# Kernel tuning notes

Hardware: AMD Instinct MI355X
Metric: run time of the kernel (lower is better)

The kernel has to match this reference:

```python
import jax, jax.numpy as jnp
import numpy as np

B, S, N, C, D = 1, 6, 10000, 128, 4
HEADS, PTS = 4, 8
HF, WF = 28, 50
M = HF * WF


def setup_inputs() -> dict:
    key0 = jax.random.key(0)
    ks = jax.random.split(key0, 14)
    sc = C ** -0.5
    d = {}
    d["query"] = jax.random.normal(ks[0], (B, N, C), jnp.float32)
    d["key"] = jax.random.normal(ks[1], (S, M, B, C), jnp.float32)
    d["value"] = jax.random.normal(ks[2], (S, M, B, C), jnp.float32)
    d["query_pos"] = jax.random.normal(ks[3], (B, N, C), jnp.float32) * 0.1
    d["reference_points_cam"] = jax.random.uniform(ks[4], (S, B, N, D, 2), jnp.float32, -0.2, 1.2)
    d["bev_mask"] = jax.random.randint(ks[5], (S, B, N, D), 0, 2).astype(bool)
    d["w_off"] = jax.random.normal(ks[6], (C, HEADS * PTS * 2), jnp.float32) * sc
    d["b_off"] = jax.random.normal(ks[7], (HEADS * PTS * 2,), jnp.float32) * 0.01
    d["w_attn"] = jax.random.normal(ks[8], (C, HEADS * PTS), jnp.float32) * sc
    d["b_attn"] = jax.random.normal(ks[9], (HEADS * PTS,), jnp.float32) * 0.01
    d["w_val"] = jax.random.normal(ks[10], (C, C), jnp.float32) * sc
    d["b_val"] = jax.random.normal(ks[11], (C,), jnp.float32) * 0.01
    d["w_out"] = jax.random.normal(ks[12], (C, C), jnp.float32) * sc
    d["b_out"] = jax.random.normal(ks[13], (C,), jnp.float32) * 0.01
    d["Hf"] = HF
    d["Wf"] = WF
    return d


def reference(query, key, value, query_pos, reference_points_cam, bev_mask,
              w_off, b_off, w_attn, b_attn, w_val, b_val, w_out, b_out, Hf, Wf):
    # SpatialCrossAttention with MSDeformAttn3D (BEVFormer semantics, eval mode: dropout=identity).
    # The torch data-dependent gather/rebatch/scatter is replaced by mathematically equivalent
    # masked computation: deformable attention is per-query independent, so running it for all
    # BEV queries per camera and mask-accumulating yields identical slots.
    B_, N_, C_ = query.shape
    S_ = key.shape[0]
    D_ = reference_points_cam.shape[3]
    H, P = HEADS, PTS
    dh = C_ // H
    Pd = P // D_
    q = query + query_pos  # (B,N,C)
    off = (q @ w_off + b_off).reshape(B_, N_, H, Pd, D_, 2)
    aw = jax.nn.softmax((q @ w_attn + b_attn).reshape(B_, N_, H, P), axis=-1)  # over levels*points (L=1)
    # value projection; per-camera feature maps laid out as (B,S,H,Hf*Wf,dh)
    v = jnp.transpose(value, (2, 0, 1, 3))  # (B,S,M,C)
    v = v @ w_val + b_val
    v = v.reshape(B_, S_, Hf * Wf, H, dh).transpose(0, 1, 3, 2, 4)  # (B,S,H,M,dh)
    ref = jnp.transpose(reference_points_cam, (1, 0, 2, 3, 4))  # (B,S,N,D,2)
    norm = jnp.array([Wf, Hf], jnp.float32)  # offset_normalizer = (W, H)
    loc = ref[:, :, :, None, None, :, :] + off[:, None] / norm  # (B,S,N,H,Pd,D,2)
    loc = loc.reshape(B_, S_, N_, H, P, 2)
    # bilinear sampling, zero padding, align_corners=False
    ix = loc[..., 0] * Wf - 0.5
    iy = loc[..., 1] * Hf - 0.5
    x0 = jnp.floor(ix)
    y0 = jnp.floor(iy)

    def flat(a):  # (B,S,N,H,P) -> (B,S,H,N*P)
        return a.transpose(0, 1, 3, 2, 4).reshape(B_, S_, H, N_ * P)

    def gather(xi, yi):
        ok = (xi >= 0) & (xi < Wf) & (yi >= 0) & (yi < Hf)
        xi_c = jnp.clip(xi, 0, Wf - 1).astype(jnp.int32)
        yi_c = jnp.clip(yi, 0, Hf - 1).astype(jnp.int32)
        idx = flat(yi_c * Wf + xi_c)
        g = jnp.take_along_axis(v, idx[..., None], axis=3)  # (B,S,H,N*P,dh)
        return g * flat(ok.astype(v.dtype))[..., None]

    wx1 = ix - x0
    wy1 = iy - y0
    wx0 = 1.0 - wx1
    wy0 = 1.0 - wy1
    samp = (gather(x0, y0) * flat(wx0 * wy0)[..., None]
            + gather(x0 + 1, y0) * flat(wx1 * wy0)[..., None]
            + gather(x0, y0 + 1) * flat(wx0 * wy1)[..., None]
            + gather(x0 + 1, y0 + 1) * flat(wx1 * wy1)[..., None])  # (B,S,H,N*P,dh)
    samp = samp.reshape(B_, S_, H, N_, P, dh)
    out = jnp.einsum('bshnpd,bnhp->bsnhd', samp, aw).reshape(B_, S_, N_, C_)
    # masked scatter-accumulate back to BEV slots
    mask = jnp.transpose(jnp.any(bev_mask, axis=-1), (1, 0, 2))  # (B,S,N)
    slots = jnp.sum(out * mask[..., None].astype(out.dtype), axis=1)  # (B,N,C)
    count = jnp.maximum(mask.astype(out.dtype).sum(axis=1), 1.0)
    slots = slots / count[..., None]
    return slots @ w_out + b_out + query  # dropout is identity in eval
```

## Files before the change

### kernel.cpp

```cpp
#include <hip/hip_runtime.h>
#include <math.h>

#define S_ 6
#define N_ 10000
#define C_ 128
#define D_ 4
#define H_ 4
#define P_ 8
#define HF_ 28
#define WF_ 50
#define M_ (HF_ * WF_)
#define DH_ 32
#define SM_ (S_ * M_)
#define ABYTES (S_ * H_ * M_ * 32)
#define VB_SH (M_ * 32)
#define CQ 64
#define NCH ((N_ + CQ - 1) / CQ)

#define NB_V ((SM_ + 31) / 32)
#define NB_O ((N_ + 31) / 32)

typedef float floatx2 __attribute__((ext_vector_type(2)));

template <int NC, int MT, int MR, int MODE>
__device__ __forceinline__ void gemm_body(
    const float* __restrict__ A, const float* __restrict__ A2,
    const float* __restrict__ B0, const float* __restrict__ B1,
    const float* __restrict__ bias0, const float* __restrict__ bias1,
    float* __restrict__ outf, char* __restrict__ out8,
    int Mrows, int m0, int tid, int nthreads, float (*Alds)[132]) {
  constexpr int NTHR = (NC / 4) * (MT / MR);

  for (int i = tid; i < MT * 32; i += nthreads) {
    int r = i >> 5, k = (i & 31) * 4;
    int row = m0 + r;
    float4 v = make_float4(0.f, 0.f, 0.f, 0.f);
    if (row < Mrows) {
      v = *(const float4*)(A + (size_t)row * C_ + k);
      if (MODE == 1) {
        float4 v2 = *(const float4*)(A2 + (size_t)row * C_ + k);
        v.x += v2.x; v.y += v2.y; v.z += v2.z; v.w += v2.w;
      }
    }
    *(float4*)(&Alds[r][k]) = v;
  }
  __syncthreads();
  if (tid >= NTHR) return;

  int ci = tid % (NC / 4);
  int mi = tid / (NC / 4);
  int c0 = ci * 4, r0 = mi * MR;

  const float* bs;
  if (MODE == 1) bs = (c0 < 64) ? bias0 + c0 : bias1 + (c0 - 64);
  else bs = bias0 + c0;

  float acc[MR][4];
#pragma unroll
  for (int j = 0; j < MR; ++j)
#pragma unroll
    for (int cc = 0; cc < 4; ++cc) acc[j][cc] = bs[cc];

#pragma unroll 2
  for (int k4 = 0; k4 < C_; k4 += 4) {
    float bf[16];
#pragma unroll
    for (int kk = 0; kk < 4; ++kk) {
      int k = k4 + kk;
      float4 b4;
      if (MODE == 1)
        b4 = (c0 < 64) ? *(const float4*)(B0 + (size_t)k * 64 + c0)
                       : *(const float4*)(B1 + (size_t)k * 32 + (c0 - 64));
      else
        b4 = *(const float4*)(B0 + (size_t)k * NC + c0);
      bf[kk * 4 + 0] = b4.x; bf[kk * 4 + 1] = b4.y;
      bf[kk * 4 + 2] = b4.z; bf[kk * 4 + 3] = b4.w;
    }
    float af[MR * 4];
#pragma unroll
    for (int j = 0; j < MR; ++j) {
      float4 a4 = *(const float4*)(&Alds[r0 + j][k4]);
      af[j * 4 + 0] = a4.x; af[j * 4 + 1] = a4.y;
      af[j * 4 + 2] = a4.z; af[j * 4 + 3] = a4.w;
    }
#pragma unroll
    for (int j = 0; j < MR; ++j)
#pragma unroll
      for (int kk = 0; kk < 4; ++kk)
#pragma unroll
        for (int cc = 0; cc < 4; ++cc)
          acc[j][cc] = fmaf(af[j * 4 + kk], bf[kk * 4 + cc], acc[j][cc]);
  }

#pragma unroll
  for (int j = 0; j < MR; ++j) {
    int row = m0 + r0 + j;
    if (row >= Mrows) continue;
    if (MODE == 0) {
      int mm = row % M_;
      int h = c0 >> 5, d0 = c0 & 31;
      int s = row / M_;
      int w = __builtin_amdgcn_cvt_pk_fp8_f32(acc[j][0], acc[j][1], 0, false);
      w = __builtin_amdgcn_cvt_pk_fp8_f32(acc[j][2], acc[j][3], w, true);
      size_t hm = (size_t)s * H_ + h;
      *(int*)(out8 + (hm * M_ + mm) * 32 + d0) = w;
    } else if (MODE == 1) {
      *(float4*)(outf + (size_t)row * 96 + c0) =
          make_float4(acc[j][0], acc[j][1], acc[j][2], acc[j][3]);
    }
  }
}

__global__ __launch_bounds__(256) void prep_kernel(
    const float* __restrict__ value, const float* __restrict__ w_val,
    const float* __restrict__ b_val, char* __restrict__ vh8,
    const float* __restrict__ query, const float* __restrict__ query_pos,
    const float* __restrict__ w_off, const float* __restrict__ b_off,
    const float* __restrict__ w_attn, const float* __restrict__ b_attn,
    float* __restrict__ OFFL) {
  __shared__ float Alds[32][132];
  int bid = blockIdx.x;
  if (bid < NB_V) {
    gemm_body<128, 32, 4, 0>(value, nullptr, w_val, nullptr, b_val, nullptr,
                             nullptr, vh8, SM_, bid * 32, threadIdx.x, 256,
                             Alds);
  } else {
    gemm_body<96, 32, 4, 1>(query, query_pos, w_off, w_attn, b_off, b_attn,
                            OFFL, nullptr, N_, (bid - NB_V) * 32, threadIdx.x,
                            256, Alds);
  }
}

__global__ __launch_bounds__(512, 4) void attn5_kernel(
    const float* __restrict__ OFFL,
    const float* __restrict__ refpts,
    const int*   __restrict__ bev_mask,
    const char*  __restrict__ wsbase,
    float* __restrict__ slot) {
  __shared__ int4 Vl4[M_ * 2];
  __shared__ int4 Pp[CQ * 9];

  int bid = blockIdx.x;
  int h = bid & 3;
  int q0 = (bid >> 2) * CQ;
  int tid = threadIdx.x;

  int tp = tid & 7, tq = tid >> 3;
  int qP = q0 + tq;
  int qPc = (qP < N_) ? qP : (N_ - 1);

  int w = tid >> 6, lane = tid & 63;
  int qg = lane >> 3, c8 = lane & 7;
  int rowsel = (c8 >> 2) & 1, xsel = (c8 >> 1) & 1, chalf = c8 & 1;
  int xsh = xsel << 4;
  int ql = w * 8 + qg;
  int qG = q0 + ql;
  int qGvalid = (qG < N_);

  float aw_p, offx, offy;
  {
    const float* lg = OFFL + (size_t)qPc * 96 + 64 + h * 8;
    float4 l0 = *(const float4*)(lg + 0);
    float4 l1 = *(const float4*)(lg + 4);
    float e[8] = {l0.x, l0.y, l0.z, l0.w, l1.x, l1.y, l1.z, l1.w};
    float mx = -1e30f;
#pragma unroll
    for (int p = 0; p < 8; ++p) mx = fmaxf(mx, e[p]);
    float sum = 0.f;
#pragma unroll
    for (int p = 0; p < 8; ++p) { e[p] = expf(e[p] - mx); sum += e[p]; }
    aw_p = e[tp] / sum;
    int pd = tp >> 2, dd = tp & 3;
    const float* ob = OFFL + (size_t)qPc * 96 + h * 16 + pd * 8 + dd * 2;
    offx = ob[0]; offy = ob[1];
  }

  floatx2 acc[8] = {{0.f, 0.f}, {0.f, 0.f}, {0.f, 0.f}, {0.f, 0.f},
                    {0.f, 0.f}, {0.f, 0.f}, {0.f, 0.f}, {0.f, 0.f}};

  for (int s = 0; s < S_; ++s) {
    __syncthreads();

    {
      const char* gsrc = wsbase + 64 + (size_t)(s * H_ + h) * VB_SH;
#pragma unroll
      for (int r = 0; r < 6; ++r) {
        int i = r * 512 + tid;
        if (i < M_ * 2) {
          __builtin_amdgcn_global_load_lds(
              (const __attribute__((address_space(1))) unsigned int*)(gsrc +
                                                                      i * 16),
              (__attribute__((address_space(3))) unsigned int*)&Vl4[i], 16, 0,
              0);
        }
      }
    }

    {
      int dd = tp & 3;
      const float* rf = refpts + ((size_t)s * N_ + qPc) * 8 + dd * 2;
      float rx = rf[0], ry = rf[1];
      const int* bm = bev_mask + ((size_t)s * N_ + qPc) * D_;
      int4 bmv = *(const int4*)bm;
      float A = ((bmv.x | bmv.y | bmv.z | bmv.w) ? 1.f : 0.f) * aw_p;
      float ix = rx * (float)WF_ + offx - 0.5f;
      float iy = ry * (float)HF_ + offy - 0.5f;
      float xf = floorf(ix), yf = floorf(iy);
      int x0 = (int)xf, y0 = (int)yf;
      float fx = ix - xf, fy = iy - yf;
      float gx = 1.f - fx, gy = 1.f - fy;
      bool vx0 = (x0 >= 0) && (x0 < WF_);
      bool vx1 = (x0 >= -1) && (x0 < WF_ - 1);
      bool vy0 = (y0 >= 0) && (y0 < HF_);
      bool vy1 = (y0 >= -1) && (y0 < HF_ - 1);
      float w00 = (vx0 && vy0) ? gx * gy * A : 0.f;
      float w10 = (vx1 && vy0) ? fx * gy * A : 0.f;
      float w01 = (vx0 && vy1) ? gx * fy * A : 0.f;
      float w11 = (vx1 && vy1) ? fx * fy * A : 0.f;
      int yt = min(max(y0, 0), HF_ - 1) * WF_;
      int yb = min(max(y0 + 1, 0), HF_ - 1) * WF_;
      int xc0 = min(max(x0, 0), WF_ - 1);
      int xc1 = min(max(x0 + 1, 0), WF_ - 1);
      int4 pk;
      pk.x = ((yt + xc0) * 2) | (((yt + xc1) * 2) << 16);
      pk.y = ((yb + xc0) * 2) | (((yb + xc1) * 2) << 16);
      union { _Float16 hf[2]; int iv; } u01, u23;
      u01.hf[0] = (_Float16)w00; u01.hf[1] = (_Float16)w10;
      u23.hf[0] = (_Float16)w01; u23.hf[1] = (_Float16)w11;
      pk.z = u01.iv;
      pk.w = u23.iv;
      Pp[tq * 9 + tp] = pk;
    }
    __syncthreads();

#pragma unroll
    for (int p = 0; p < 8; ++p) {
      int4 prm = Pp[ql * 9 + p];
      int vword = rowsel ? prm.y : prm.x;
      int vidx = (int)(((unsigned)vword >> xsh) & 0xffffu);
      int wword = rowsel ? prm.w : prm.z;
      union { unsigned short u; _Float16 hf; } cu;
      cu.u = (unsigned short)((unsigned)wword >> xsh);
      float wgt = (float)cu.hf;
      int4 tv = Vl4[vidx + chalf];
      floatx2 wv = {wgt, wgt};
      acc[0] += __builtin_amdgcn_cvt_pk_f32_fp8(tv.x, false) * wv;
      acc[1] += __builtin_amdgcn_cvt_pk_f32_fp8(tv.x, true)  * wv;
      acc[2] += __builtin_amdgcn_cvt_pk_f32_fp8(tv.y, false) * wv;
      acc[3] += __builtin_amdgcn_cvt_pk_f32_fp8(tv.y, true)  * wv;
      acc[4] += __builtin_amdgcn_cvt_pk_f32_fp8(tv.z, false) * wv;
      acc[5] += __builtin_amdgcn_cvt_pk_f32_fp8(tv.z, true)  * wv;
      acc[6] += __builtin_amdgcn_cvt_pk_f32_fp8(tv.w, false) * wv;
      acc[7] += __builtin_amdgcn_cvt_pk_f32_fp8(tv.w, true)  * wv;
    }
  }

  float av[16];
#pragma unroll
  for (int k = 0; k < 8; ++k) { av[2 * k] = acc[k][0]; av[2 * k + 1] = acc[k][1]; }
#pragma unroll
  for (int k = 0; k < 16; ++k) av[k] += __shfl_xor(av[k], 2);
#pragma unroll
  for (int k = 0; k < 16; ++k) av[k] += __shfl_xor(av[k], 4);

  if (c8 < 2 && qGvalid) {
    int cnt = 0;
#pragma unroll
    for (int s = 0; s < S_; ++s) {
      const int* bm = bev_mask + ((size_t)s * N_ + qG) * D_;
      int4 bmv = *(const int4*)bm;
      cnt += (bmv.x | bmv.y | bmv.z | bmv.w) ? 1 : 0;
    }
    float inv = 1.f / (float)(cnt > 0 ? cnt : 1);
    float* dst = slot + (size_t)qG * C_ + h * DH_ + chalf * 16;
    *(float4*)(dst + 0)  = make_float4(av[0] * inv, av[1] * inv, av[2] * inv, av[3] * inv);
    *(float4*)(dst + 4)  = make_float4(av[4] * inv, av[5] * inv, av[6] * inv, av[7] * inv);
    *(float4*)(dst + 8)  = make_float4(av[8] * inv, av[9] * inv, av[10] * inv, av[11] * inv);
    *(float4*)(dst + 12) = make_float4(av[12] * inv, av[13] * inv, av[14] * inv, av[15] * inv);
  }
}

__global__ __launch_bounds__(256) void outproj_kernel(
    const float* __restrict__ slot, const float* __restrict__ query,
    const float* __restrict__ w_out, const float* __restrict__ b_out,
    float* __restrict__ out) {
  __shared__ float slds[32][132];
  int q0 = blockIdx.x * 32, tid = threadIdx.x;

  for (int i = tid; i < 32 * 32; i += 256) {
    int r = i >> 5, k = (i & 31) * 4;
    int qc = min(q0 + r, N_ - 1);
    *(float4*)(&slds[r][k]) = *(const float4*)(slot + (size_t)qc * C_ + k);
  }
  __syncthreads();

  {
    int ci = tid & 31, mi = tid >> 5;
    int c0 = ci * 4, r0 = mi * 4;
    float acc[4][4];
#pragma unroll
    for (int j = 0; j < 4; ++j) {
      int qq = min(q0 + r0 + j, N_ - 1);
      float4 qv = *(const float4*)(query + (size_t)qq * C_ + c0);
      float4 bv = *(const float4*)(b_out + c0);
      acc[j][0] = bv.x + qv.x; acc[j][1] = bv.y + qv.y;
      acc[j][2] = bv.z + qv.z; acc[j][3] = bv.w + qv.w;
    }
#pragma unroll 2
    for (int k4 = 0; k4 < C_; k4 += 4) {
      float bf[16];
#pragma unroll
      for (int kk = 0; kk < 4; ++kk) {
        float4 b4 = *(const float4*)(w_out + (size_t)(k4 + kk) * C_ + c0);
        bf[kk * 4 + 0] = b4.x; bf[kk * 4 + 1] = b4.y;
        bf[kk * 4 + 2] = b4.z; bf[kk * 4 + 3] = b4.w;
      }
      float af[16];
#pragma unroll
      for (int j = 0; j < 4; ++j) {
        float4 a4 = *(const float4*)(&slds[r0 + j][k4]);
        af[j * 4 + 0] = a4.x; af[j * 4 + 1] = a4.y;
        af[j * 4 + 2] = a4.z; af[j * 4 + 3] = a4.w;
      }
#pragma unroll
      for (int j = 0; j < 4; ++j)
#pragma unroll
        for (int kk = 0; kk < 4; ++kk)
#pragma unroll
          for (int cc = 0; cc < 4; ++cc)
            acc[j][cc] = fmaf(af[j * 4 + kk], bf[kk * 4 + cc], acc[j][cc]);
    }
#pragma unroll
    for (int j = 0; j < 4; ++j) {
      int qq = q0 + r0 + j;
      if (qq < N_)
        *(float4*)(out + (size_t)qq * C_ + c0) =
            make_float4(acc[j][0], acc[j][1], acc[j][2], acc[j][3]);
    }
  }
}

extern "C" void kernel_launch(void* const* d_in, const int* in_sizes, int n_in,
                              void* d_out, int out_size, void* d_ws, size_t ws_size,
                              hipStream_t stream) {
  const float* query     = (const float*)d_in[0];
  const float* value     = (const float*)d_in[2];
  const float* query_pos = (const float*)d_in[3];
  const float* refpts    = (const float*)d_in[4];
  const int*   bev_mask  = (const int*)d_in[5];
  const float* w_off     = (const float*)d_in[6];
  const float* b_off     = (const float*)d_in[7];
  const float* w_attn    = (const float*)d_in[8];
  const float* b_attn    = (const float*)d_in[9];
  const float* w_val     = (const float*)d_in[10];
  const float* b_val     = (const float*)d_in[11];
  const float* w_out     = (const float*)d_in[12];
  const float* b_out     = (const float*)d_in[13];

  char* ws = (char*)d_ws;
  char* vh8   = ws + 64;
  float* OFFL = (float*)(ws + 64 + 2 * (size_t)ABYTES + 64);
  float* SLOT = (float*)(ws + 64 + 2 * (size_t)ABYTES + 64 +
                         (size_t)N_ * 96 * 4);

  prep_kernel<<<NB_V + NB_O, 256, 0, stream>>>(
      value, w_val, b_val, vh8, query, query_pos, w_off, b_off, w_attn, b_attn,
      OFFL);
  attn5_kernel<<<NCH * H_, 512, 0, stream>>>(OFFL, refpts, bev_mask, ws, SLOT);
  outproj_kernel<<<(N_ + 31) / 32, 256, 0, stream>>>(SLOT, query, w_out, b_out,
                                                     (float*)d_out);
}
```

Before: 158.3 us.

## Double-buffer per-camera value staging and split channel halves across blocks

Restructures the attention kernel so each block handles one channel half of one head, with 256 threads instead of 512. Camera feature maps and packed sample parameters are double-buffered in LDS, so the next camera's global-to-LDS load and parameter computation overlap with the current camera's accumulation, removing one barrier per iteration. The cost is twice as many blocks, each recomputing the softmax and offsets for its queries, along with strided 16-byte loads and a different shuffle reduction. The smaller per-block LDS staging may also change occupancy.

```diff
diff --git a/kernel.cpp b/kernel.cpp
--- a/kernel.cpp
+++ b/kernel.cpp
@@ -131,143 +131,173 @@
   }
 }
 
-__global__ __launch_bounds__(512, 4) void attn5_kernel(
+__global__ __launch_bounds__(256, 2) void attn6_kernel(
     const float* __restrict__ OFFL,
     const float* __restrict__ refpts,
     const int*   __restrict__ bev_mask,
     const char*  __restrict__ wsbase,
     float* __restrict__ slot) {
-  __shared__ int4 Vl4[M_ * 2];
-  __shared__ int4 Pp[CQ * 9];
+  __shared__ int4 Vbuf[2][M_];
+  __shared__ int4 Pp[2][CQ * 9];
 
   int bid = blockIdx.x;
-  int h = bid & 3;
-  int q0 = (bid >> 2) * CQ;
+  int chalf = bid & 1;
+  int h = (bid >> 1) & 3;
+  int q0 = (bid >> 3) * CQ;
   int tid = threadIdx.x;
 
-  int tp = tid & 7, tq = tid >> 3;
-  int qP = q0 + tq;
-  int qPc = (qP < N_) ? qP : (N_ - 1);
-
   int w = tid >> 6, lane = tid & 63;
-  int qg = lane >> 3, c8 = lane & 7;
-  int rowsel = (c8 >> 2) & 1, xsel = (c8 >> 1) & 1, chalf = c8 & 1;
+  int role = lane & 3, ql16 = lane >> 2;
+  int rowsel = role >> 1, xsel = role & 1;
   int xsh = xsel << 4;
-  int ql = w * 8 + qg;
-  int qG = q0 + ql;
-  int qGvalid = (qG < N_);
-
-  float aw_p, offx, offy;
+  int qlG = w * 16 + ql16;
+  int qG = q0 + qlG;
+  bool qGv = (qG < N_);
+  int qGc = qGv ? qG : (N_ - 1);
+
+  int pA = tid & 7, qA = tid >> 3;
+  int gqA = min(q0 + qA, N_ - 1);
+  int gqB = min(q0 + qA + 32, N_ - 1);
+
+  float awA, oxA, oyA, awB, oxB, oyB;
   {
-    const float* lg = OFFL + (size_t)qPc * 96 + 64 + h * 8;
-    float4 l0 = *(const float4*)(lg + 0);
-    float4 l1 = *(const float4*)(lg + 4);
-    float e[8] = {l0.x, l0.y, l0.z, l0.w, l1.x, l1.y, l1.z, l1.w};
+    const float* lg = OFFL + (size_t)gqA * 96 + 64 + h * 8;
+    float e[8];
     float mx = -1e30f;
 #pragma unroll
-    for (int p = 0; p < 8; ++p) mx = fmaxf(mx, e[p]);
+    for (int p = 0; p < 8; ++p) { e[p] = lg[p]; mx = fmaxf(mx, e[p]); }
     float sum = 0.f;
 #pragma unroll
     for (int p = 0; p < 8; ++p) { e[p] = expf(e[p] - mx); sum += e[p]; }
-    aw_p = e[tp] / sum;
-    int pd = tp >> 2, dd = tp & 3;
-    const float* ob = OFFL + (size_t)qPc * 96 + h * 16 + pd * 8 + dd * 2;
-    offx = ob[0]; offy = ob[1];
-  }
+    awA = e[pA] / sum;
+    int pd = pA >> 2, dd = pA & 3;
+    const float* ob = OFFL + (size_t)gqA * 96 + h * 16 + pd * 8 + dd * 2;
+    oxA = ob[0]; oyA = ob[1];
+  }
+  {
+    const float* lg = OFFL + (size_t)gqB * 96 + 64 + h * 8;
+    float e[8];
+    float mx = -1e30f;
+#pragma unroll
+    for (int p = 0; p < 8; ++p) { e[p] = lg[p]; mx = fmaxf(mx, e[p]); }
+    float sum = 0.f;
+#pragma unroll
+    for (int p = 0; p < 8; ++p) { e[p] = expf(e[p] - mx); sum += e[p]; }
+    awB = e[pA] / sum;
+    int pd = pA >> 2, dd = pA & 3;
+    const float* ob = OFFL + (size_t)gqB * 96 + h * 16 + pd * 8 + dd * 2;
+    oxB = ob[0]; oyB = ob[1];
+  }
+
+  auto stage = [&](int s) {
+    int b = s & 1;
+    const char* gsrc = wsbase + 64 + (size_t)(s * H_ + h) * VB_SH + chalf * 16;
+#pragma unroll
+    for (int r = 0; r < 6; ++r) {
+      int i = r * 256 + tid;
+      if (i < M_) {
+        __builtin_amdgcn_global_load_lds(
+            (const __attribute__((address_space(1))) unsigned int*)(gsrc +
+                                                                    (size_t)i *
+                                                                        32),
+            (__attribute__((address_space(3))) unsigned int*)&Vbuf[b][i], 16,
+            0, 0);
+      }
+    }
+  };
+
+  auto psample = [&](int s, int b, int gq, int qloc, int p, float aw, float ox,
+                     float oy) {
+    int dd = p & 3;
+    const float* rf = refpts + ((size_t)s * N_ + gq) * 8 + dd * 2;
+    float rx = rf[0], ry = rf[1];
+    const int* bm = bev_mask + ((size_t)s * N_ + gq) * D_;
+    int4 bmv = *(const int4*)bm;
+    float A = ((bmv.x | bmv.y | bmv.z | bmv.w) ? 1.f : 0.f) * aw;
+    float ix = rx * (float)WF_ + ox - 0.5f;
+    float iy = ry * (float)HF_ + oy - 0.5f;
+    float xf = floorf(ix), yf = floorf(iy);
+    int x0 = (int)xf, y0 = (int)yf;
+    float fx = ix - xf, fy = iy - yf;
+    float gx = 1.f - fx, gy = 1.f - fy;
+    bool vx0 = (x0 >= 0) && (x0 < WF_);
+    bool vx1 = (x0 >= -1) && (x0 < WF_ - 1);
+    bool vy0 = (y0 >= 0) && (y0 < HF_);
+    bool vy1 = (y0 >= -1) && (y0 < HF_ - 1);
+    float w00 = (vx0 && vy0) ? gx * gy * A : 0.f;
+    float w10 = (vx1 && vy0) ? fx * gy * A : 0.f;
+    float w01 = (vx0 && vy1) ? gx * fy * A : 0.f;
+    float w11 = (vx1 && vy1) ? fx * fy * A : 0.f;
+    int yt = min(max(y0, 0), HF_ - 1) * WF_;
+    int yb = min(max(y0 + 1, 0), HF_ - 1) * WF_;
+    int xc0 = min(max(x0, 0), WF_ - 1);
+    int xc1 = min(max(x0 + 1, 0), WF_ - 1);
+    int4 pk;
+    pk.x = (yt + xc0) | ((yt + xc1) << 16);
+    pk.y = (yb + xc0) | ((yb + xc1) << 16);
+    union { _Float16 hf[2]; int iv; } u01, u23;
+    u01.hf[0] = (_Float16)w00; u01.hf[1] = (_Float16)w10;
+    u23.hf[0] = (_Float16)w01; u23.hf[1] = (_Float16)w11;
+    pk.z = u01.iv;
+    pk.w = u23.iv;
+    Pp[b][qloc * 9 + p] = pk;
+  };
 
   floatx2 acc[8] = {{0.f, 0.f}, {0.f, 0.f}, {0.f, 0.f}, {0.f, 0.f},
                     {0.f, 0.f}, {0.f, 0.f}, {0.f, 0.f}, {0.f, 0.f}};
 
+  stage(0);
+  psample(0, 0, gqA, qA, pA, awA, oxA, oyA);
+  psample(0, 0, gqB, qA + 32, pA, awB, oxB, oyB);
+  __syncthreads();
+
   for (int s = 0; s < S_; ++s) {
+    if (s + 1 < S_) {
+      stage(s + 1);
+      psample(s + 1, (s + 1) & 1, gqA, qA, pA, awA, oxA, oyA);
+      psample(s + 1, (s + 1) & 1, gqB, qA + 32, pA, awB, oxB, oyB);
+    }
+    {
+      int b = s & 1;
+      const int4* pp = &Pp[b][qlG * 9];
+      const int4* vb = Vbuf[b];
+#pragma unroll
+      for (int p = 0; p < 8; ++p) {
+        int4 prm = pp[p];
+        int vword = rowsel ? prm.y : prm.x;
+        int pix = (int)(((unsigned)vword >> xsh) & 0xffffu);
+        int wword = rowsel ? prm.w : prm.z;
+        union { unsigned short u; _Float16 hf; } cu;
+        cu.u = (unsigned short)((unsigned)wword >> xsh);
+        float wgt = (float)cu.hf;
+        int4 tv = vb[pix];
+        floatx2 wv = {wgt, wgt};
+        acc[0] += __builtin_amdgcn_cvt_pk_f32_fp8(tv.x, false) * wv;
+        acc[1] += __builtin_amdgcn_cvt_pk_f32_fp8(tv.x, true)  * wv;
+        acc[2] += __builtin_amdgcn_cvt_pk_f32_fp8(tv.y, false) * wv;
+        acc[3] += __builtin_amdgcn_cvt_pk_f32_fp8(tv.y, true)  * wv;
+        acc[4] += __builtin_amdgcn_cvt_pk_f32_fp8(tv.z, false) * wv;
+        acc[5] += __builtin_amdgcn_cvt_pk_f32_fp8(tv.z, true)  * wv;
+        acc[6] += __builtin_amdgcn_cvt_pk_f32_fp8(tv.w, false) * wv;
+        acc[7] += __builtin_amdgcn_cvt_pk_f32_fp8(tv.w, true)  * wv;
+      }
+    }
     __syncthreads();
-
-    {
-      const char* gsrc = wsbase + 64 + (size_t)(s * H_ + h) * VB_SH;
-#pragma unroll
-      for (int r = 0; r < 6; ++r) {
-        int i = r * 512 + tid;
-        if (i < M_ * 2) {
-          __builtin_amdgcn_global_load_lds(
-              (const __attribute__((address_space(1))) unsigned int*)(gsrc +
-                                                                      i * 16),
-              (__attribute__((address_space(3))) unsigned int*)&Vl4[i], 16, 0,
-              0);
-        }
-      }
-    }
-
-    {
-      int dd = tp & 3;
-      const float* rf = refpts + ((size_t)s * N_ + qPc) * 8 + dd * 2;
-      float rx = rf[0], ry = rf[1];
-      const int* bm = bev_mask + ((size_t)s * N_ + qPc) * D_;
-      int4 bmv = *(const int4*)bm;
-      float A = ((bmv.x | bmv.y | bmv.z | bmv.w) ? 1.f : 0.f) * aw_p;
-      float ix = rx * (float)WF_ + offx - 0.5f;
-      float iy = ry * (float)HF_ + offy - 0.5f;
-      float xf = floorf(ix), yf = floorf(iy);
-      int x0 = (int)xf, y0 = (int)yf;
-      float fx = ix - xf, fy = iy - yf;
-      float gx = 1.f - fx, gy = 1.f - fy;
-      bool vx0 = (x0 >= 0) && (x0 < WF_);
-      bool vx1 = (x0 >= -1) && (x0 < WF_ - 1);
-      bool vy0 = (y0 >= 0) && (y0 < HF_);
-      bool vy1 = (y0 >= -1) && (y0 < HF_ - 1);
-      float w00 = (vx0 && vy0) ? gx * gy * A : 0.f;
-      float w10 = (vx1 && vy0) ? fx * gy * A : 0.f;
-      float w01 = (vx0 && vy1) ? gx * fy * A : 0.f;
-      float w11 = (vx1 && vy1) ? fx * fy * A : 0.f;
-      int yt = min(max(y0, 0), HF_ - 1) * WF_;
-      int yb = min(max(y0 + 1, 0), HF_ - 1) * WF_;
-      int xc0 = min(max(x0, 0), WF_ - 1);
-      int xc1 = min(max(x0 + 1, 0), WF_ - 1);
-      int4 pk;
-      pk.x = ((yt + xc0) * 2) | (((yt + xc1) * 2) << 16);
-      pk.y = ((yb + xc0) * 2) | (((yb + xc1) * 2) << 16);
-      union { _Float16 hf[2]; int iv; } u01, u23;
-      u01.hf[0] = (_Float16)w00; u01.hf[1] = (_Float16)w10;
-      u23.hf[0] = (_Float16)w01; u23.hf[1] = (_Float16)w11;
-      pk.z = u01.iv;
-      pk.w = u23.iv;
-      Pp[tq * 9 + tp] = pk;
-    }
-    __syncthreads();
-
-#pragma unroll
-    for (int p = 0; p < 8; ++p) {
-      int4 prm = Pp[ql * 9 + p];
-      int vword = rowsel ? prm.y : prm.x;
-      int vidx = (int)(((unsigned)vword >> xsh) & 0xffffu);
-      int wword = rowsel ? prm.w : prm.z;
-      union { unsigned short u; _Float16 hf; } cu;
-      cu.u = (unsigned short)((unsigned)wword >> xsh);
-      float wgt = (float)cu.hf;
-      int4 tv = Vl4[vidx + chalf];
-      floatx2 wv = {wgt, wgt};
-      acc[0] += __builtin_amdgcn_cvt_pk_f32_fp8(tv.x, false) * wv;
-      acc[1] += __builtin_amdgcn_cvt_pk_f32_fp8(tv.x, true)  * wv;
-      acc[2] += __builtin_amdgcn_cvt_pk_f32_fp8(tv.y, false) * wv;
-      acc[3] += __builtin_amdgcn_cvt_pk_f32_fp8(tv.y, true)  * wv;
-      acc[4] += __builtin_amdgcn_cvt_pk_f32_fp8(tv.z, false) * wv;
-      acc[5] += __builtin_amdgcn_cvt_pk_f32_fp8(tv.z, true)  * wv;
-      acc[6] += __builtin_amdgcn_cvt_pk_f32_fp8(tv.w, false) * wv;
-      acc[7] += __builtin_amdgcn_cvt_pk_f32_fp8(tv.w, true)  * wv;
-    }
   }
 
   float av[16];
 #pragma unroll
   for (int k = 0; k < 8; ++k) { av[2 * k] = acc[k][0]; av[2 * k + 1] = acc[k][1]; }
 #pragma unroll
+  for (int k = 0; k < 16; ++k) av[k] += __shfl_xor(av[k], 1);
+#pragma unroll
   for (int k = 0; k < 16; ++k) av[k] += __shfl_xor(av[k], 2);
-#pragma unroll
-  for (int k = 0; k < 16; ++k) av[k] += __shfl_xor(av[k], 4);
-
-  if (c8 < 2 && qGvalid) {
+
+  if (role == 0 && qGv) {
     int cnt = 0;
 #pragma unroll
     for (int s = 0; s < S_; ++s) {
-      const int* bm = bev_mask + ((size_t)s * N_ + qG) * D_;
+      const int* bm = bev_mask + ((size_t)s * N_ + qGc) * D_;
       int4 bmv = *(const int4*)bm;
       cnt += (bmv.x | bmv.y | bmv.z | bmv.w) ? 1 : 0;
     }
@@ -366,7 +396,8 @@
   prep_kernel<<<NB_V + NB_O, 256, 0, stream>>>(
       value, w_val, b_val, vh8, query, query_pos, w_off, b_off, w_attn, b_attn,
       OFFL);
-  attn5_kernel<<<NCH * H_, 512, 0, stream>>>(OFFL, refpts, bev_mask, ws, SLOT);
+  attn6_kernel<<<NCH * H_ * 2, 256, 0, stream>>>(OFFL, refpts, bev_mask, ws,
+                                                 SLOT);
   outproj_kernel<<<(N_ + 31) / 32, 256, 0, stream>>>(SLOT, query, w_out, b_out,
                                                      (float*)d_out);
 }
```

Result: slower. 165.2 us (+4.3%).
